# Performance work log

Measured on AMD Instinct MI355X. Metric: run time of the kernel, lower is better.

## Reference

```python
import jax, jax.numpy as jnp
import numpy as np

D_MODEL = 1024
N_HEADS = 16
D_K = D_MODEL // N_HEADS


def setup_inputs() -> dict:
    key = jax.random.key(0)
    ks = jax.random.split(key, 12)
    B, S = 4, 2048
    s = 1.0 / np.sqrt(D_MODEL)
    return {
        "query": jax.random.normal(ks[0], (B, S, D_MODEL), jnp.float32),
        "key": jax.random.normal(ks[1], (B, S, D_MODEL), jnp.float32),
        "value": jax.random.normal(ks[2], (B, S, D_MODEL), jnp.float32),
        "Wq": jax.random.normal(ks[3], (D_MODEL, D_MODEL), jnp.float32) * s,
        "bq": jnp.zeros((D_MODEL,), jnp.float32),
        "Wk": jax.random.normal(ks[4], (D_MODEL, D_MODEL), jnp.float32) * s,
        "bk": jnp.zeros((D_MODEL,), jnp.float32),
        "Wv": jax.random.normal(ks[5], (D_MODEL, D_MODEL), jnp.float32) * s,
        "bv": jnp.zeros((D_MODEL,), jnp.float32),
        "Wo": jax.random.normal(ks[6], (D_MODEL, D_MODEL), jnp.float32) * s,
        "bo": jnp.zeros((D_MODEL,), jnp.float32),
    }


def reference(query, key, value, Wq, bq, Wk, bk, Wv, bv, Wo, bo):
    B, S, _ = query.shape

    def shape(x):  # [B,S,D] -> [B,H,S,d_k]
        return x.reshape(B, -1, N_HEADS, D_K).transpose(0, 2, 1, 3)

    q = shape(query @ Wq + bq)
    k = shape(key @ Wk + bk)
    v = shape(value @ Wv + bv)
    scores = jnp.einsum("bhqd,bhkd->bhqk", q, k) / jnp.sqrt(jnp.float32(D_K))
    p_attn = jax.nn.softmax(scores, axis=-1)  # dropout p=0 -> identity
    x = jnp.einsum("bhqk,bhkd->bhqd", p_attn, v)
    x = x.transpose(0, 2, 1, 3).reshape(B, -1, N_HEADS * D_K)
    return x @ Wo + bo
```

## Files before the change

kernel.cpp:

```cpp
#include <hip/hip_runtime.h>

typedef __bf16 bf16x8 __attribute__((ext_vector_type(8)));
typedef float f32x4 __attribute__((ext_vector_type(4)));
typedef float f32x16 __attribute__((ext_vector_type(16)));
typedef unsigned int u32x4v __attribute__((ext_vector_type(4)));
typedef unsigned short ushort_t;


__device__ __forceinline__ unsigned short f2bf(float f) {
    unsigned int u = __builtin_bit_cast(unsigned int, f);
    u += 0x7FFFu + ((u >> 16) & 1u);
    return (unsigned short)(u >> 16);
}

__device__ __forceinline__ unsigned int cvtpk(float lo, float hi) {
    unsigned int r;
    asm("v_cvt_pk_bf16_f32 %0, %1, %2" : "=v"(r) : "v"(lo), "v"(hi));
    return r;
}

__device__ __forceinline__ void async16(const void* g, void* l) {
    __builtin_amdgcn_global_load_lds(
        (const __attribute__((address_space(1))) void*)g,
        (__attribute__((address_space(3))) void*)l, 16, 0, 0);
}

#define MFMA16(a, b, c) __builtin_amdgcn_mfma_f32_16x16x32_bf16((a), (b), (c), 0, 0, 0)
#define MFMA32(a, b, c) __builtin_amdgcn_mfma_f32_32x32x16_bf16((a), (b), (c), 0, 0, 0)


__global__ void __launch_bounds__(256)
castk3(const float* __restrict__ a, const float* __restrict__ b, const float* __restrict__ c,
       ushort_t* __restrict__ oa, ushort_t* __restrict__ ob, ushort_t* __restrict__ oc, int n8) {
    int i = blockIdx.x * blockDim.x + threadIdx.x;
    int stride = gridDim.x * blockDim.x;
    for (; i < 3 * n8; i += stride) {
        const float* in; ushort_t* out; int j = i;
        if (j < n8)            { in = a; out = oa; }
        else if (j < 2 * n8)   { in = b; out = ob; j -= n8; }
        else                   { in = c; out = oc; j -= 2 * n8; }
        const float4* p = (const float4*)(in + (size_t)j * 8);
        float4 x = p[0], y = p[1];
        ushort_t r[8] = { f2bf(x.x), f2bf(x.y), f2bf(x.z), f2bf(x.w),
                          f2bf(y.x), f2bf(y.y), f2bf(y.z), f2bf(y.w) };
        *(uint4*)(out + (size_t)j * 8) = *(uint4*)r;
    }
}


__global__ void __launch_bounds__(256)
wtrans4(const float* __restrict__ W0, const float* __restrict__ W1,
        const float* __restrict__ W2, const float* __restrict__ W3,
        ushort_t* __restrict__ T0, ushort_t* __restrict__ T1,
        ushort_t* __restrict__ T2, ushort_t* __restrict__ T3) {
    __shared__ __attribute__((aligned(16))) float t[64][72];
    int z = blockIdx.z;
    const float* W = z == 0 ? W0 : z == 1 ? W1 : z == 2 ? W2 : W3;
    ushort_t* Wt   = z == 0 ? T0 : z == 1 ? T1 : z == 2 ? T2 : T3;
    int k0 = blockIdx.x * 64, n0 = blockIdx.y * 64;
    int tid = threadIdx.x;
#pragma unroll
    for (int i = 0; i < 4; ++i) {
        int ci = i * 256 + tid;
        int r = ci >> 4, c4 = (ci & 15) * 4;
        *(float4*)&t[r][c4] = *(const float4*)&W[(size_t)(k0 + r) * 1024 + n0 + c4];
    }
    __syncthreads();
#pragma unroll
    for (int i = 0; i < 2; ++i) {
        int ci = i * 256 + tid;
        int n = ci & 63, kb = ci >> 6;
        ushort_t tmp[8];
#pragma unroll
        for (int j = 0; j < 8; ++j) tmp[j] = f2bf(t[kb * 8 + j][n]);
        *(uint4*)&Wt[(size_t)(n0 + n) * 1024 + k0 + kb * 8] = *(uint4*)tmp;
    }
}


__global__ void __launch_bounds__(256)
vtrans(const ushort_t* __restrict__ V, ushort_t* __restrict__ Vt) {
    __shared__ __attribute__((aligned(16))) ushort_t t[64][80];
    int bh = blockIdx.x, st = blockIdx.y;
    const ushort_t* src = V + ((size_t)bh * 2048 + st * 64) * 64;
    int tid = threadIdx.x;
#pragma unroll
    for (int i = 0; i < 2; ++i) {
        int c = i * 256 + tid;
        int r = c >> 3, col = (c & 7) * 8;
        *(uint4*)&t[r][col] = *(const uint4*)&src[(size_t)r * 64 + col];
    }
    __syncthreads();
    ushort_t* dst = Vt + (size_t)bh * 64 * 2048 + st * 64;
#pragma unroll
    for (int i = 0; i < 2; ++i) {
        int c = i * 256 + tid;
        int d = c & 63, sb = c >> 6;
        ushort_t tmp[8];
#pragma unroll
        for (int j = 0; j < 8; ++j) tmp[j] = t[sb * 8 + j][d];
        *(uint4*)&dst[(size_t)d * 2048 + sb * 8] = *(uint4*)tmp;
    }
}


__global__ void __launch_bounds__(256)
proj_qkv(const ushort_t* __restrict__ Xq, const ushort_t* __restrict__ Xk,
         const ushort_t* __restrict__ Xv, const ushort_t* __restrict__ Wt,
         const float* __restrict__ bqp, const float* __restrict__ bkp,
         const float* __restrict__ bvp,
         ushort_t* __restrict__ Qp, ushort_t* __restrict__ Kp, ushort_t* __restrict__ Vp) {
    __shared__ __attribute__((aligned(16))) ushort_t lA[128 * 64];
    __shared__ __attribute__((aligned(16))) ushort_t lB[128 * 64];
    const int tid = threadIdx.x;
    const int wave = tid >> 6, lane = tid & 63;
    const int lr = lane & 15, lg = lane >> 4;
    const int wm = wave >> 1, wn = wave & 1;
    const size_t m0 = (size_t)blockIdx.x * 128;
    const int sel = blockIdx.y >> 3;
    const int n0 = (blockIdx.y & 7) * 128;

    const ushort_t* A    = sel == 0 ? Xq : sel == 1 ? Xk : Xv;
    const ushort_t* Bt   = Wt + (size_t)sel * 1024 * 1024;
    const float*    bias = sel == 0 ? bqp : sel == 1 ? bkp : bvp;
    ushort_t*       dst  = sel == 0 ? Qp : sel == 1 ? Kp : Vp;
    const float     scale = sel == 0 ? 0.125f : 1.0f;

    f32x4 acc[4][4] = {};

    for (int kt = 0; kt < 16; ++kt) {
        __syncthreads();
#pragma unroll
        for (int i = 0; i < 4; ++i) {
            int c = i * 256 + tid;
            int r = c >> 3;
            int sc = (c & 7) ^ (r & 7);
            async16(A + (m0 + r) * 1024 + kt * 64 + sc * 8, &lA[(i * 256 + wave * 64) * 8]);
        }
#pragma unroll
        for (int i = 0; i < 4; ++i) {
            int c = i * 256 + tid;
            int r = c >> 3;
            int sc = (c & 7) ^ (r & 7);
            async16(Bt + (size_t)(n0 + r) * 1024 + kt * 64 + sc * 8, &lB[(i * 256 + wave * 64) * 8]);
        }
        __syncthreads();
#pragma unroll
        for (int kc = 0; kc < 2; ++kc) {
            bf16x8 af[4], bfr[4];
#pragma unroll
            for (int t = 0; t < 4; ++t) {
                int rowA = wm * 64 + t * 16 + lr;
                int byteA = (rowA * 128 + (kc * 32 + lg * 8) * 2) ^ ((rowA & 7) << 4);
                af[t] = *(const bf16x8*)((const char*)lA + byteA);
                int rowB = wn * 64 + t * 16 + lr;
                int byteB = (rowB * 128 + (kc * 32 + lg * 8) * 2) ^ ((rowB & 7) << 4);
                bfr[t] = *(const bf16x8*)((const char*)lB + byteB);
            }
#pragma unroll
            for (int i = 0; i < 4; ++i)
#pragma unroll
                for (int j = 0; j < 4; ++j)
                    acc[i][j] = MFMA16(af[i], bfr[j], acc[i][j]);
        }
    }

    float bv[4];
#pragma unroll
    for (int nt = 0; nt < 4; ++nt) bv[nt] = bias[n0 + wn * 64 + nt * 16 + lr];

#pragma unroll
    for (int mt = 0; mt < 4; ++mt)
#pragma unroll
        for (int nt = 0; nt < 4; ++nt)
#pragma unroll
            for (int j = 0; j < 4; ++j) {
                size_t m = m0 + wm * 64 + mt * 16 + lg * 4 + j;
                int n = n0 + wn * 64 + nt * 16 + lr;
                size_t b = m >> 11, s = m & 2047;
                int h = n >> 6, dk = n & 63;
                float v = (acc[mt][nt][j] + bv[nt]) * scale;
                dst[((b * 16 + h) * 2048 + s) * 64 + dk] = f2bf(v);
            }
}


__global__ void __launch_bounds__(256)
gemm_out(const ushort_t* __restrict__ A, const ushort_t* __restrict__ Bt,
         const float* __restrict__ bias, float* __restrict__ dst) {
    __shared__ __attribute__((aligned(16))) ushort_t lA[128 * 64];
    __shared__ __attribute__((aligned(16))) ushort_t lB[128 * 64];
    const int tid = threadIdx.x;
    const int wave = tid >> 6, lane = tid & 63;
    const int lr = lane & 15, lg = lane >> 4;
    const int wm = wave >> 1, wn = wave & 1;
    const size_t m0 = (size_t)blockIdx.x * 128;
    const int n0 = blockIdx.y * 128;

    f32x4 acc[4][4] = {};

    for (int kt = 0; kt < 16; ++kt) {
        __syncthreads();
#pragma unroll
        for (int i = 0; i < 4; ++i) {
            int c = i * 256 + tid;
            int r = c >> 3;
            int sc = (c & 7) ^ (r & 7);
            async16(A + (m0 + r) * 1024 + kt * 64 + sc * 8, &lA[(i * 256 + wave * 64) * 8]);
        }
#pragma unroll
        for (int i = 0; i < 4; ++i) {
            int c = i * 256 + tid;
            int r = c >> 3;
            int sc = (c & 7) ^ (r & 7);
            async16(Bt + (size_t)(n0 + r) * 1024 + kt * 64 + sc * 8, &lB[(i * 256 + wave * 64) * 8]);
        }
        __syncthreads();
#pragma unroll
        for (int kc = 0; kc < 2; ++kc) {
            bf16x8 af[4], bfr[4];
#pragma unroll
            for (int t = 0; t < 4; ++t) {
                int rowA = wm * 64 + t * 16 + lr;
                int byteA = (rowA * 128 + (kc * 32 + lg * 8) * 2) ^ ((rowA & 7) << 4);
                af[t] = *(const bf16x8*)((const char*)lA + byteA);
                int rowB = wn * 64 + t * 16 + lr;
                int byteB = (rowB * 128 + (kc * 32 + lg * 8) * 2) ^ ((rowB & 7) << 4);
                bfr[t] = *(const bf16x8*)((const char*)lB + byteB);
            }
#pragma unroll
            for (int i = 0; i < 4; ++i)
#pragma unroll
                for (int j = 0; j < 4; ++j)
                    acc[i][j] = MFMA16(af[i], bfr[j], acc[i][j]);
        }
    }

    float bv[4];
#pragma unroll
    for (int nt = 0; nt < 4; ++nt) bv[nt] = bias[n0 + wn * 64 + nt * 16 + lr];

#pragma unroll
    for (int mt = 0; mt < 4; ++mt)
#pragma unroll
        for (int nt = 0; nt < 4; ++nt)
#pragma unroll
            for (int j = 0; j < 4; ++j) {
                size_t m = m0 + wm * 64 + mt * 16 + lg * 4 + j;
                int n = n0 + wn * 64 + nt * 16 + lr;
                dst[m * 1024 + n] = acc[mt][nt][j] + bv[nt];
            }
}


__global__ void __launch_bounds__(256)
attn(const ushort_t* __restrict__ Q, const ushort_t* __restrict__ Kb,
     const ushort_t* __restrict__ Vt, ushort_t* __restrict__ X) {
    __shared__ __attribute__((aligned(16))) ushort_t lK[64 * 64];
    __shared__ __attribute__((aligned(16))) ushort_t lV[64 * 64];
    const int tid = threadIdx.x, wave = tid >> 6, lane = tid & 63;
    const int ql = lane & 31, hi = lane >> 5;
    const int bh = blockIdx.x;
    const int q0 = blockIdx.y * 128 + wave * 32;

    const ushort_t* Qg = Q + ((size_t)bh * 2048 + q0 + ql) * 64 + hi * 8;
    bf16x8 qf[4];
#pragma unroll
    for (int dk = 0; dk < 4; ++dk) qf[dk] = *(const bf16x8*)(Qg + dk * 16);

    const int rx = ql & 7;
    int off[4];
#pragma unroll
    for (int dk = 0; dk < 4; ++dk) off[dk] = ((dk * 2 + hi) ^ rx) * 16;
    const char* kB0 = (const char*)lK + ql * 128;
    const char* kB1 = kB0 + 32 * 128;
    const char* vB0 = (const char*)lV + ql * 128;
    const char* vB1 = vB0 + 32 * 128;

    int sr[2], ssc[2];
#pragma unroll
    for (int i = 0; i < 2; ++i) {
        int c = i * 256 + tid;
        sr[i] = c >> 3;
        ssc[i] = (c & 7) ^ (sr[i] & 7);
    }
    const ushort_t* Kroot = Kb + (size_t)bh * 2048 * 64;
    const ushort_t* Vroot = Vt + (size_t)bh * 64 * 2048;

    f32x16 oa0 = {}, oa1 = {};
    float mrun = -1e30f, lrun = 0.f;

    for (int kv0 = 0; kv0 < 2048; kv0 += 64) {
        __syncthreads();
#pragma unroll
        for (int i = 0; i < 2; ++i)
            async16(Kroot + (size_t)(kv0 + sr[i]) * 64 + ssc[i] * 8,
                    &lK[(i * 256 + wave * 64) * 8]);
#pragma unroll
        for (int i = 0; i < 2; ++i)
            async16(Vroot + (size_t)sr[i] * 2048 + kv0 + ssc[i] * 8,
                    &lV[(i * 256 + wave * 64) * 8]);
        __syncthreads();

        f32x16 st0 = {}, st1 = {};
#pragma unroll
        for (int dk = 0; dk < 4; ++dk) {
            bf16x8 k0 = *(const bf16x8*)(kB0 + off[dk]);
            bf16x8 k1 = *(const bf16x8*)(kB1 + off[dk]);
            st0 = MFMA32(k0, qf[dk], st0);
            st1 = MFMA32(k1, qf[dk], st1);
        }

        float mloc = st0[0];
#pragma unroll
        for (int r = 1; r < 16; ++r) mloc = fmaxf(mloc, st0[r]);
#pragma unroll
        for (int r = 0; r < 16; ++r) mloc = fmaxf(mloc, st1[r]);
        float mx = fmaxf(mloc, __shfl_xor(mloc, 32));
        float mnew = fmaxf(mrun, mx);
        float scl = __expf(mrun - mnew);
        mrun = mnew;
        float ps = 0.f;
#pragma unroll
        for (int r = 0; r < 16; ++r) { float e = __expf(st0[r] - mnew); st0[r] = e; ps += e; }
#pragma unroll
        for (int r = 0; r < 16; ++r) { float e = __expf(st1[r] - mnew); st1[r] = e; ps += e; }
        lrun = lrun * scl + ps;
#pragma unroll
        for (int r = 0; r < 16; ++r) { oa0[r] *= scl; oa1[r] *= scl; }

        bf16x8 pb[4];
#pragma unroll
        for (int ks = 0; ks < 4; ++ks) {
            int rb = (ks & 1) * 8;
            unsigned int A_, B_, C_, D_;
            if (ks < 2) {
                A_ = cvtpk(st0[rb + 0], st0[rb + 1]);
                B_ = cvtpk(st0[rb + 4], st0[rb + 5]);
                C_ = cvtpk(st0[rb + 2], st0[rb + 3]);
                D_ = cvtpk(st0[rb + 6], st0[rb + 7]);
            } else {
                A_ = cvtpk(st1[rb + 0], st1[rb + 1]);
                B_ = cvtpk(st1[rb + 4], st1[rb + 5]);
                C_ = cvtpk(st1[rb + 2], st1[rb + 3]);
                D_ = cvtpk(st1[rb + 6], st1[rb + 7]);
            }
            asm("v_permlane32_swap_b32 %0, %1" : "+v"(A_), "+v"(B_));
            asm("v_permlane32_swap_b32 %0, %1" : "+v"(C_), "+v"(D_));
            u32x4v w = { A_, C_, B_, D_ };
            pb[ks] = __builtin_bit_cast(bf16x8, w);
        }

#pragma unroll
        for (int ks = 0; ks < 4; ++ks) {
            bf16x8 v0 = *(const bf16x8*)(vB0 + off[ks]);
            bf16x8 v1 = *(const bf16x8*)(vB1 + off[ks]);
            oa0 = MFMA32(v0, pb[ks], oa0);
            oa1 = MFMA32(v1, pb[ks], oa1);
        }
    }

    float lt = lrun + __shfl_xor(lrun, 32);
    float inv = 1.f / lt;
    const int b = bh >> 4, h = bh & 15;
    ushort_t* dst = X + (((size_t)b * 2048 + q0 + ql) * 16 + h) * 64;
#pragma unroll
    for (int rq = 0; rq < 4; ++rq) {
        ushort_t t0[4], t1[4];
#pragma unroll
        for (int j = 0; j < 4; ++j) {
            t0[j] = f2bf(oa0[rq * 4 + j] * inv);
            t1[j] = f2bf(oa1[rq * 4 + j] * inv);
        }
        *(ushort4*)(dst + rq * 8 + hi * 4)      = *(ushort4*)t0;
        *(ushort4*)(dst + 32 + rq * 8 + hi * 4) = *(ushort4*)t1;
    }
}


extern "C" void kernel_launch(void* const* d_in, const int* in_sizes, int n_in,
                              void* d_out, int out_size, void* d_ws, size_t ws_size,
                              hipStream_t stream) {
    const float* query = (const float*)d_in[0];
    const float* key   = (const float*)d_in[1];
    const float* value = (const float*)d_in[2];
    const float* Wq = (const float*)d_in[3];
    const float* bq = (const float*)d_in[4];
    const float* Wk = (const float*)d_in[5];
    const float* bk = (const float*)d_in[6];
    const float* Wv = (const float*)d_in[7];
    const float* bv = (const float*)d_in[8];
    const float* Wo = (const float*)d_in[9];
    const float* bo = (const float*)d_in[10];
    float* out = (float*)d_out;

    char* ws = (char*)d_ws;
    const size_t MB = 1024 * 1024;
    ushort_t* Wqt = (ushort_t*)(ws + 0 * MB);
    ushort_t* Wkt = (ushort_t*)(ws + 2 * MB);
    ushort_t* Wvt = (ushort_t*)(ws + 4 * MB);
    ushort_t* Wot = (ushort_t*)(ws + 6 * MB);
    ushort_t* Xq  = (ushort_t*)(ws + 8 * MB);
    ushort_t* Xk  = (ushort_t*)(ws + 24 * MB);
    ushort_t* Xv  = (ushort_t*)(ws + 40 * MB);
    ushort_t* Qp  = (ushort_t*)(ws + 56 * MB);
    ushort_t* Kp  = (ushort_t*)(ws + 72 * MB);
    ushort_t* Vp  = (ushort_t*)(ws + 88 * MB);
    ushort_t* Vtp = Xq;
    ushort_t* Xat = Xk;

    const int n8 = 8192 * 1024 / 8;
    castk3<<<dim3(2048), dim3(256), 0, stream>>>(query, key, value, Xq, Xk, Xv, n8);

    wtrans4<<<dim3(16, 16, 4), dim3(256), 0, stream>>>(Wq, Wk, Wv, Wo, Wqt, Wkt, Wvt, Wot);

    proj_qkv<<<dim3(64, 24), dim3(256), 0, stream>>>(Xq, Xk, Xv, Wqt, bq, bk, bv, Qp, Kp, Vp);

    vtrans<<<dim3(64, 32), dim3(256), 0, stream>>>(Vp, Vtp);

    attn<<<dim3(64, 16), dim3(256), 0, stream>>>(Qp, Kp, Vtp, Xat);

    gemm_out<<<dim3(64, 8), dim3(256), 0, stream>>>(Xat, Wot, bo, out);
}
```

Before: 374.2 us.

## Double-buffer K/V tiles and use lazy exp2 rescaling in attention

The attention kernel now keeps two LDS buffers for K and V and prefetches the next tile asynchronously while the current one is computed, waiting with a partial vmcnt instead of a full barrier before each load. The softmax switches to exp2 by folding log2(e) into the Q scale, uses tree reductions for max and sum, and only rescales the accumulators when the running max rises by more than a threshold. It also raises wave priority around the MFMA sections. Together these aim to hide global-memory latency and cut the VALU work in the softmax, at the cost of twice the LDS per block and reliance on the skipped-rescale bound to avoid overflow.

```diff
diff --git a/kernel.cpp b/kernel.cpp
--- a/kernel.cpp
+++ b/kernel.cpp
@@ -124,7 +124,7 @@
     const ushort_t* Bt   = Wt + (size_t)sel * 1024 * 1024;
     const float*    bias = sel == 0 ? bqp : sel == 1 ? bkp : bvp;
     ushort_t*       dst  = sel == 0 ? Qp : sel == 1 ? Kp : Vp;
-    const float     scale = sel == 0 ? 0.125f : 1.0f;
+    const float     scale = sel == 0 ? 0.18033688f : 1.0f;
 
     f32x4 acc[4][4] = {};
 
@@ -256,8 +256,8 @@
 __global__ void __launch_bounds__(256)
 attn(const ushort_t* __restrict__ Q, const ushort_t* __restrict__ Kb,
      const ushort_t* __restrict__ Vt, ushort_t* __restrict__ X) {
-    __shared__ __attribute__((aligned(16))) ushort_t lK[64 * 64];
-    __shared__ __attribute__((aligned(16))) ushort_t lV[64 * 64];
+    __shared__ __attribute__((aligned(16))) ushort_t lK[2][64 * 64];
+    __shared__ __attribute__((aligned(16))) ushort_t lV[2][64 * 64];
     const int tid = threadIdx.x, wave = tid >> 6, lane = tid & 63;
     const int ql = lane & 31, hi = lane >> 5;
     const int bh = blockIdx.x;
@@ -272,10 +272,7 @@
     int off[4];
 #pragma unroll
     for (int dk = 0; dk < 4; ++dk) off[dk] = ((dk * 2 + hi) ^ rx) * 16;
-    const char* kB0 = (const char*)lK + ql * 128;
-    const char* kB1 = kB0 + 32 * 128;
-    const char* vB0 = (const char*)lV + ql * 128;
-    const char* vB1 = vB0 + 32 * 128;
+    const int rowb = ql * 128;
 
     int sr[2], ssc[2];
 #pragma unroll
@@ -287,47 +284,72 @@
     const ushort_t* Kroot = Kb + (size_t)bh * 2048 * 64;
     const ushort_t* Vroot = Vt + (size_t)bh * 64 * 2048;
 
+    auto stage = [&](int tile, int bi) {
+        int kv0 = tile * 64;
+#pragma unroll
+        for (int i = 0; i < 2; ++i)
+            async16(Kroot + (size_t)(kv0 + sr[i]) * 64 + ssc[i] * 8,
+                    &lK[bi][(i * 256 + wave * 64) * 8]);
+#pragma unroll
+        for (int i = 0; i < 2; ++i)
+            async16(Vroot + (size_t)sr[i] * 2048 + kv0 + ssc[i] * 8,
+                    &lV[bi][(i * 256 + wave * 64) * 8]);
+    };
+
     f32x16 oa0 = {}, oa1 = {};
     float mrun = -1e30f, lrun = 0.f;
 
-    for (int kv0 = 0; kv0 < 2048; kv0 += 64) {
-        __syncthreads();
-#pragma unroll
-        for (int i = 0; i < 2; ++i)
-            async16(Kroot + (size_t)(kv0 + sr[i]) * 64 + ssc[i] * 8,
-                    &lK[(i * 256 + wave * 64) * 8]);
-#pragma unroll
-        for (int i = 0; i < 2; ++i)
-            async16(Vroot + (size_t)sr[i] * 2048 + kv0 + ssc[i] * 8,
-                    &lV[(i * 256 + wave * 64) * 8]);
-        __syncthreads();
+    stage(0, 0);
+    for (int t = 0; t < 32; ++t) {
+        const int cur = t & 1;
+        stage((t + 1) & 31, cur ^ 1);
+        asm volatile("s_waitcnt vmcnt(4)" ::: "memory");
+        __builtin_amdgcn_s_barrier();
+
+        const char* kB0 = (const char*)&lK[cur][0] + rowb;
+        const char* vB0 = (const char*)&lV[cur][0] + rowb;
 
         f32x16 st0 = {}, st1 = {};
+        __builtin_amdgcn_s_setprio(1);
 #pragma unroll
         for (int dk = 0; dk < 4; ++dk) {
             bf16x8 k0 = *(const bf16x8*)(kB0 + off[dk]);
-            bf16x8 k1 = *(const bf16x8*)(kB1 + off[dk]);
+            bf16x8 k1 = *(const bf16x8*)(kB0 + 32 * 128 + off[dk]);
             st0 = MFMA32(k0, qf[dk], st0);
             st1 = MFMA32(k1, qf[dk], st1);
         }
-
-        float mloc = st0[0];
-#pragma unroll
-        for (int r = 1; r < 16; ++r) mloc = fmaxf(mloc, st0[r]);
-#pragma unroll
-        for (int r = 0; r < 16; ++r) mloc = fmaxf(mloc, st1[r]);
-        float mx = fmaxf(mloc, __shfl_xor(mloc, 32));
-        float mnew = fmaxf(mrun, mx);
-        float scl = __expf(mrun - mnew);
-        mrun = mnew;
-        float ps = 0.f;
-#pragma unroll
-        for (int r = 0; r < 16; ++r) { float e = __expf(st0[r] - mnew); st0[r] = e; ps += e; }
-#pragma unroll
-        for (int r = 0; r < 16; ++r) { float e = __expf(st1[r] - mnew); st1[r] = e; ps += e; }
-        lrun = lrun * scl + ps;
-#pragma unroll
-        for (int r = 0; r < 16; ++r) { oa0[r] *= scl; oa1[r] *= scl; }
+        __builtin_amdgcn_s_setprio(0);
+
+        float tm[16];
+#pragma unroll
+        for (int r = 0; r < 16; ++r) tm[r] = fmaxf(st0[r], st1[r]);
+#pragma unroll
+        for (int s = 8; s > 0; s >>= 1)
+#pragma unroll
+            for (int r = 0; r < s; ++r) tm[r] = fmaxf(tm[r], tm[r + s]);
+        float mx = fmaxf(tm[0], __shfl_xor(tm[0], 32));
+
+        if (!__all(mx - mrun <= 8.f)) {
+            float mnew = fmaxf(mrun, mx);
+            float scl = __builtin_amdgcn_exp2f(mrun - mnew);
+            mrun = mnew;
+            lrun *= scl;
+#pragma unroll
+            for (int r = 0; r < 16; ++r) { oa0[r] *= scl; oa1[r] *= scl; }
+        }
+
+#pragma unroll
+        for (int r = 0; r < 16; ++r) st0[r] = __builtin_amdgcn_exp2f(st0[r] - mrun);
+#pragma unroll
+        for (int r = 0; r < 16; ++r) st1[r] = __builtin_amdgcn_exp2f(st1[r] - mrun);
+        float sa[8];
+#pragma unroll
+        for (int r = 0; r < 8; ++r) sa[r] = (st0[r] + st0[r + 8]) + (st1[r] + st1[r + 8]);
+#pragma unroll
+        for (int s = 4; s > 0; s >>= 1)
+#pragma unroll
+            for (int r = 0; r < s; ++r) sa[r] += sa[r + s];
+        lrun += sa[0];
 
         bf16x8 pb[4];
 #pragma unroll
@@ -351,13 +373,17 @@
             pb[ks] = __builtin_bit_cast(bf16x8, w);
         }
 
+        __builtin_amdgcn_s_setprio(1);
 #pragma unroll
         for (int ks = 0; ks < 4; ++ks) {
             bf16x8 v0 = *(const bf16x8*)(vB0 + off[ks]);
-            bf16x8 v1 = *(const bf16x8*)(vB1 + off[ks]);
+            bf16x8 v1 = *(const bf16x8*)(vB0 + 32 * 128 + off[ks]);
             oa0 = MFMA32(v0, pb[ks], oa0);
             oa1 = MFMA32(v1, pb[ks], oa1);
         }
+        __builtin_amdgcn_s_setprio(0);
+
+        __builtin_amdgcn_s_barrier();
     }
 
     float lt = lrun + __shfl_xor(lrun, 32);
```

After: 382.1 us. +2.1%, slower.
